# Kernel optimization log

Hardware: AMD Instinct MI355X
Metric: run time of the kernel (lower is better)

The kernel has to match this reference:

```python
import jax, jax.numpy as jnp
import numpy as np

C = 64        # channels
D = 64        # dense grid side at tensor_stride 1
N = 100000    # active voxels


def _conv3d(x, w, stride, pad):
    # x: (D,D,D,Cin), w: (kd,kh,kw,Cin,Cout) -> (D',D',D',Cout)
    return jax.lax.conv_general_dilated(
        x[None], w, window_strides=(stride,) * 3, padding=pad,
        dimension_numbers=('NDHWC', 'DHWIO', 'NDHWC'))[0]


def _sconv(x, w, b, mask, stride=1, pad='SAME'):
    # Minkowski sparse conv == dense conv on zero-filled grid, restricted to
    # the active output sites (bias only added at active sites).
    return (_conv3d(x, w, stride, pad) + b) * mask


def _forward(coords, coords_ds, feats_c1, feats_ref, w_fuse, b_fuse, w_down, b_down,
             w_conv2, b_conv2, w_p00, b_p00, w_p01, b_p01, w_p10, b_p10,
             w_p11, b_p11, w_p12, b_p12):
    dt = feats_c1.dtype
    Dh = D // 2
    ci, cj, ck = coords[:, 0], coords[:, 1], coords[:, 2]
    di, dj, dk = coords_ds[:, 0], coords_ds[:, 1], coords_ds[:, 2]
    mask = jnp.zeros((D, D, D, 1), dt).at[ci, cj, ck, 0].set(1.0)
    mask_ds = jnp.zeros((Dh, Dh, Dh, 1), dt).at[di, dj, dk, 0].set(1.0)
    fused = jnp.concatenate([feats_c1, feats_ref], axis=1)            # (N, 2C)
    x = jnp.zeros((D, D, D, 2 * C), dt).at[ci, cj, ck].set(fused)
    x = jax.nn.relu(_sconv(x, w_fuse, b_fuse, mask))                  # conv_fuse, k=3 s=1
    x = jax.nn.relu(_sconv(x, w_down, b_down, mask_ds, stride=2, pad='VALID'))  # conv_down1, k=2 s=2
    x = _sconv(x, w_conv2, b_conv2, mask_ds)                          # conv_2, no relu
    for i in range(w_p00.shape[0]):                                   # InceptionResNet x3
        p0 = jax.nn.relu(_sconv(x, w_p00[i], b_p00[i], mask_ds))      # k3 C->C/4
        p0 = _sconv(p0, w_p01[i], b_p01[i], mask_ds)                  # k3 C/4->C/2
        p1 = jax.nn.relu(_sconv(x, w_p10[i], b_p10[i], mask_ds))      # k1 C->C/4
        p1 = jax.nn.relu(_sconv(p1, w_p11[i], b_p11[i], mask_ds))     # k3 C/4->C/4
        p1 = _sconv(p1, w_p12[i], b_p12[i], mask_ds)                  # k1 C/4->C/2
        x = jnp.concatenate([p0, p1], axis=-1) + x                    # cat + residual
    return x[di, dj, dk]                                              # (M, C) sparse output feats


def setup_inputs() -> dict:
    rng = np.random.default_rng(0)
    flat = rng.choice(D ** 3, size=N, replace=False)                  # unique occupied voxels
    coords = np.stack(np.unravel_index(flat, (D, D, D)), axis=1).astype(np.int32)
    coords_ds = np.unique(coords // 2, axis=0).astype(np.int32)       # stride-2 active set
    key = jax.random.key(0)
    ks = iter(jax.random.split(key, 40))

    def W(shape, fan_in):
        return jax.random.normal(next(ks), shape, jnp.float32) / np.float32(np.sqrt(fan_in))

    def B(shape):
        return jax.random.normal(next(ks), shape, jnp.float32) * 0.01

    L = 3  # res blocks
    return dict(
        coords=jnp.asarray(coords), coords_ds=jnp.asarray(coords_ds),
        feats_c1=jax.random.normal(next(ks), (N, C), jnp.float32),
        feats_ref=jax.random.normal(next(ks), (N, C), jnp.float32),
        w_fuse=W((3, 3, 3, 2 * C, C), 27 * 2 * C), b_fuse=B((C,)),
        w_down=W((2, 2, 2, C, C), 8 * C), b_down=B((C,)),
        w_conv2=W((3, 3, 3, C, C), 27 * C), b_conv2=B((C,)),
        w_p00=W((L, 3, 3, 3, C, C // 4), 27 * C), b_p00=B((L, C // 4)),
        w_p01=W((L, 3, 3, 3, C // 4, C // 2), 27 * C // 4), b_p01=B((L, C // 2)),
        w_p10=W((L, 1, 1, 1, C, C // 4), C), b_p10=B((L, C // 4)),
        w_p11=W((L, 3, 3, 3, C // 4, C // 4), 27 * C // 4), b_p11=B((L, C // 4)),
        w_p12=W((L, 1, 1, 1, C // 4, C // 2), C // 4), b_p12=B((L, C // 2)),
    )


def reference(coords, coords_ds, feats_c1, feats_ref, w_fuse, b_fuse, w_down, b_down,
              w_conv2, b_conv2, w_p00, b_p00, w_p01, b_p01, w_p10, b_p10,
              w_p11, b_p11, w_p12, b_p12):
    return _forward(coords, coords_ds, feats_c1, feats_ref, w_fuse, b_fuse, w_down,
                    b_down, w_conv2, b_conv2, w_p00, b_p00, w_p01, b_p01, w_p10,
                    b_p10, w_p11, b_p11, w_p12, b_p12)
```

## Files before the change

kernel.cpp:

```cpp
#include <hip/hip_runtime.h>

#define GD 64
#define GDS 32

typedef _Float16 f16;
typedef __attribute__((ext_vector_type(8))) _Float16 f16x8;
typedef __attribute__((ext_vector_type(4))) float f32x4;

#define GLOAD_LDS16(SRC, DST)                                                        \
    __builtin_amdgcn_global_load_lds(                                                \
        (const __attribute__((address_space(1))) unsigned int*)(const void*)(SRC),   \
        (__attribute__((address_space(3))) unsigned int*)(void*)(DST), 16, 0, 0)

__global__ __launch_bounds__(256) void init_kernel(int* __restrict__ idx_grid,
                                                   unsigned char* __restrict__ ds_mask,
                                                   f16* __restrict__ zrow,
                                                   f16* __restrict__ f1z) {
    int i = blockIdx.x * 256 + threadIdx.x;
    if (i < GD * GD * GD) idx_grid[i] = -1;
    if (i < GDS * GDS * GDS) ds_mask[i] = 0;
    if (i < 128) zrow[i] = (f16)0.f;
    if (i < 64) f1z[i] = (f16)0.f;
}

__global__ __launch_bounds__(256) void scatter_kernel(const int* __restrict__ coords, int N,
                                                      const int* __restrict__ coords_ds, int M,
                                                      int* __restrict__ idx_grid,
                                                      unsigned char* __restrict__ ds_mask) {
    int i = blockIdx.x * 256 + threadIdx.x;
    if (i < N) {
        int a = coords[i * 3], b = coords[i * 3 + 1], c = coords[i * 3 + 2];
        idx_grid[(a * GD + b) * GD + c] = i;
    }
    if (i < M) {
        int a = coords_ds[i * 3], b = coords_ds[i * 3 + 1], c = coords_ds[i * 3 + 2];
        ds_mask[(a * GDS + b) * GDS + c] = 1;
    }
}

__global__ __launch_bounds__(256) void count_kernel(const int* __restrict__ idx_grid,
                                                    int* __restrict__ cnt) {
    __shared__ int c;
    if (threadIdx.x == 0) c = 0;
    __syncthreads();
    int s = blockIdx.x * 256 + threadIdx.x;
    bool act = idx_grid[s] >= 0;
    unsigned long long m = __ballot(act);
    if ((threadIdx.x & 63) == 0) atomicAdd(&c, __popcll(m));
    __syncthreads();
    if (threadIdx.x == 0) cnt[blockIdx.x] = c;
}

__global__ __launch_bounds__(1024) void prefix_kernel(const int* __restrict__ cnt,
                                                      int* __restrict__ off) {
    __shared__ int s[1024];
    int t = threadIdx.x;
    int v0 = cnt[t];
    s[t] = v0;
    __syncthreads();
    for (int d = 1; d < 1024; d <<= 1) {
        int v = 0;
        if (t >= d) v = s[t - d];
        __syncthreads();
        s[t] += v;
        __syncthreads();
    }
    off[t] = s[t] - v0;
}

__global__ __launch_bounds__(256) void emit_kernel(int* __restrict__ idx_grid,
                                                   const int* __restrict__ off,
                                                   int* __restrict__ sites,
                                                   int* __restrict__ perm) {
    int tid = threadIdx.x, bid = blockIdx.x;
    int s = bid * 256 + tid;
    int orig = idx_grid[s];
    bool act = orig >= 0;
    unsigned long long m = __ballot(act);
    int lane = tid & 63, wv = tid >> 6;
    __shared__ int wcnt[4];
    if (lane == 0) wcnt[wv] = __popcll(m);
    __syncthreads();
    int base = off[bid];
    for (int w = 0; w < wv; ++w) base += wcnt[w];
    int rank = __popcll(m & ((1ull << lane) - 1ull));
    if (act) {
        int q = base + rank;
        sites[q] = s;
        perm[q] = orig;
        idx_grid[s] = q;
    }
}

__global__ __launch_bounds__(256) void pack_kernel(
    const float* __restrict__ wf, const float* __restrict__ wd, const float* __restrict__ wc2,
    const float* __restrict__ wp00, const float* __restrict__ wp01, const float* __restrict__ wp10,
    const float* __restrict__ wp11, const float* __restrict__ wp12, const float* __restrict__ bp00,
    const float* __restrict__ bp01, const float* __restrict__ bp10, const float* __restrict__ bp11,
    int L, f16* __restrict__ wc1, f16* __restrict__ wdnh, f16* __restrict__ wc2h,
    f16* __restrict__ wfA, f16* __restrict__ wfB, f16* __restrict__ w12h, float* __restrict__ bA,
    float* __restrict__ bB) {
    int i = blockIdx.x * 256 + threadIdx.x;
    int n;
    n = 27 * 8192;
    if (i < n) {
        int tap = i >> 13, oc = (i >> 7) & 63, ic = i & 127;
        wc1[i] = (f16)wf[(tap * 128 + ic) * 64 + oc];
        return;
    }
    i -= n;
    n = 8 * 4096;
    if (i < n) {
        int t = i >> 12, oc = (i >> 6) & 63, ic = i & 63;
        wdnh[i] = (f16)wd[(t * 64 + ic) * 64 + oc];
        return;
    }
    i -= n;
    n = 27 * 4096;
    if (i < n) {
        int tap = i >> 12, oc = (i >> 6) & 63, ic = i & 63;
        wc2h[i] = (f16)wc2[(tap * 64 + ic) * 64 + oc];
        return;
    }
    i -= n;
    n = L * 27 * 2048;
    if (i < n) {
        int l = i / (27 * 2048), r = i - l * 27 * 2048;
        int tap = r >> 11, oc = (r >> 6) & 31, ic = r & 63;
        float v = 0.f;
        if (oc < 16) v = wp00[(((size_t)l * 27 + tap) * 64 + ic) * 16 + oc];
        else if (tap == 13) v = wp10[((size_t)l * 64 + ic) * 16 + (oc - 16)];
        wfA[i] = (f16)v;
        return;
    }
    i -= n;
    n = L * 27 * 1536;
    if (i < n) {
        int l = i / (27 * 1536), r = i - l * 27 * 1536;
        int tap = r / 1536, q = r - tap * 1536;
        int oc = q >> 5, ic = q & 31;
        float v = 0.f;
        if (oc < 32) {
            if (ic < 16) v = wp01[(((size_t)l * 27 + tap) * 16 + ic) * 32 + oc];
        } else {
            if (ic >= 16) v = wp11[(((size_t)l * 27 + tap) * 16 + (ic - 16)) * 16 + (oc - 32)];
        }
        wfB[i] = (f16)v;
        return;
    }
    i -= n;
    n = L * 512;
    if (i < n) {
        int l = i >> 9, q = i & 511, oc = q >> 4, ic = q & 15;
        w12h[i] = (f16)wp12[((size_t)l * 16 + ic) * 32 + oc];
        return;
    }
    i -= n;
    n = L * 32;
    if (i < n) {
        int l = i >> 5, oc = i & 31;
        bA[i] = (oc < 16) ? bp00[l * 16 + oc] : bp10[l * 16 + oc - 16];
        return;
    }
    i -= n;
    n = L * 48;
    if (i < n) {
        int l = i / 48, c = i - l * 48;
        bB[i] = (c < 32) ? bp01[l * 32 + c] : bp11[l * 16 + (c - 32)];
    }
}

__global__ __launch_bounds__(256) void fusef_kernel(const float* __restrict__ fc1,
                                                    const float* __restrict__ fref,
                                                    const int* __restrict__ perm, int N,
                                                    f16* __restrict__ feats) {
    int i = blockIdx.x * 256 + threadIdx.x;
    if (i < (N + 1) * 128) {
        int q = i >> 7, c = i & 127;
        float v = 0.f;
        if (q < N) {
            int p = perm[q];
            v = (c < 64) ? fc1[p * 64 + c] : fref[p * 64 + c - 64];
        }
        feats[i] = (f16)v;
    }
}

__global__ __launch_bounds__(256) void conv1_pipe(const int* __restrict__ sites,
                                                  const int* __restrict__ idx_grid, int N,
                                                  const f16* __restrict__ featsB,
                                                  const f16* __restrict__ wc1,
                                                  const float* __restrict__ bias,
                                                  f16* __restrict__ out ) {
    __shared__ f16 xb[2][64 * 128];
    __shared__ f16 wb[2][64 * 128];
    __shared__ int nbr[64 * 27];
    const int tid = threadIdx.x;
    const int nwg = gridDim.x, orig = blockIdx.x;
    const int qq = nwg >> 3, rr2 = nwg & 7;
    const int xcd = orig & 7, sub = orig >> 3;
    const int wg = (xcd < rr2 ? xcd * (qq + 1) : rr2 * (qq + 1) + (xcd - rr2) * qq) + sub;
    const int q0 = wg * 64;

    for (int t = tid; t < 64 * 27; t += 256) {
        int p = t / 27, tap = t - p * 27;
        int q = q0 + p, nb = N;
        if (q < N) {
            int s = sites[q];
            int i = (s >> 12) + tap / 9 - 1;
            int j = ((s >> 6) & 63) + (tap / 3) % 3 - 1;
            int k = (s & 63) + tap % 3 - 1;
            if ((unsigned)i < 64u && (unsigned)j < 64u && (unsigned)k < 64u) {
                int r = idx_grid[(i << 12) + (j << 6) + k];
                if (r >= 0) nb = r;
            }
        }
        nbr[t] = nb;
    }
    __syncthreads();

    const int lane = tid & 63, wid = tid >> 6;
    const int l16 = lane & 15, lq = lane >> 4;
    const int m0 = (wid >> 1) * 32, n0 = (wid & 1) * 32;

    auto STAGE = [&](int tap, int buf) {
#pragma unroll
        for (int r = 0; r < 4; ++r) {
            int slot = r * 256 + tid;
            int row = slot >> 4, cl = slot & 15;
            int c = cl ^ (row & 15);
            const f16* src = featsB + (size_t)nbr[row * 27 + tap] * 128 + c * 8;
            GLOAD_LDS16(src, &xb[buf][0] + (size_t)(r * 256 + (tid & ~63)) * 8);
        }
#pragma unroll
        for (int r = 0; r < 4; ++r) {
            int slot = r * 256 + tid;
            int row = slot >> 4, cl = slot & 15;
            int c = cl ^ (row & 15);
            const f16* src = wc1 + (size_t)((tap * 64 + row) * 128 + c * 8);
            GLOAD_LDS16(src, &wb[buf][0] + (size_t)(r * 256 + (tid & ~63)) * 8);
        }
    };

    f32x4 acc[2][2] = {};
    STAGE(0, 0);
    STAGE(1, 1);
    for (int tap = 0; tap < 27; ++tap) {
        if (tap < 26) {
            asm volatile("s_waitcnt vmcnt(8)" ::: "memory");
        } else {
            asm volatile("s_waitcnt vmcnt(0)" ::: "memory");
        }
        __builtin_amdgcn_sched_barrier(0);
        __builtin_amdgcn_s_barrier();

        const f16* xp = &xb[tap & 1][0];
        const f16* wp = &wb[tap & 1][0];
        f16x8 a[2][4], b[2][4];
#pragma unroll
        for (int mi = 0; mi < 2; ++mi) {
            int row = m0 + mi * 16 + l16;
#pragma unroll
            for (int ks = 0; ks < 4; ++ks)
                a[mi][ks] =
                    *(const f16x8*)(xp + (size_t)row * 128 + (size_t)((((ks * 4 + lq) ^ l16)) * 8));
        }
#pragma unroll
        for (int ni = 0; ni < 2; ++ni) {
            int col = n0 + ni * 16 + l16;
#pragma unroll
            for (int ks = 0; ks < 4; ++ks)
                b[ni][ks] =
                    *(const f16x8*)(wp + (size_t)col * 128 + (size_t)((((ks * 4 + lq) ^ l16)) * 8));
        }
#pragma unroll
        for (int mi = 0; mi < 2; ++mi)
#pragma unroll
            for (int ni = 0; ni < 2; ++ni)
#pragma unroll
                for (int ks = 0; ks < 4; ++ks)
                    acc[mi][ni] = __builtin_amdgcn_mfma_f32_16x16x32_f16(a[mi][ks], b[ni][ks],
                                                                         acc[mi][ni], 0, 0, 0);
        asm volatile("s_waitcnt lgkmcnt(0)" ::: "memory");
        __builtin_amdgcn_sched_barrier(0);
        __builtin_amdgcn_s_barrier();
        if (tap + 2 < 27) STAGE(tap + 2, tap & 1);
    }

#pragma unroll
    for (int ni = 0; ni < 2; ++ni) {
        int col = n0 + ni * 16 + l16;
        float bv = bias[col];
#pragma unroll
        for (int mi = 0; mi < 2; ++mi) {
#pragma unroll
            for (int j = 0; j < 4; ++j) {
                int q = q0 + m0 + mi * 16 + lq * 4 + j;
                if (q < N) {
                    float v = acc[mi][ni][j] + bv;
                    out[(size_t)q * 64 + col] = (f16)(v > 0.f ? v : 0.f);
                }
            }
        }
    }
}

__global__ __launch_bounds__(512) void down_mfma(const f16* __restrict__ feats1h, int N,
                                                 const int* __restrict__ idx_grid,
                                                 const f16* __restrict__ wdn,
                                                 const float* __restrict__ bias,
                                                 const unsigned char* __restrict__ mask,
                                                 f16* __restrict__ out ) {
    __shared__ f16 xs[2][128 * 64];
    __shared__ f16 wl[2][512 * 8];
    __shared__ int nbr[128 * 8];
    const int tid = threadIdx.x;
    const int s0 = blockIdx.x * 128;
    for (int t = tid; t < 128 * 8; t += 512) {
        int sl = t >> 3, tp = t & 7;
        int s = s0 + sl;
        int i = s >> 10, j = (s >> 5) & 31, k = s & 31;
        int ci = 2 * i + (tp >> 2), cj = 2 * j + ((tp >> 1) & 1), ck = 2 * k + (tp & 1);
        int r = idx_grid[(ci * GD + cj) * GD + ck];
        nbr[t] = (r >= 0) ? r : N;
    }
    __syncthreads();
    auto STAGEX = [&](int tp, int buf) {
#pragma unroll
        for (int rr = 0; rr < 2; ++rr) {
            int slot = rr * 512 + tid;
            int row = slot >> 3, cl = slot & 7;
            int c = cl ^ (row & 7);
            const f16* src = feats1h + (size_t)nbr[row * 8 + tp] * 64 + c * 8;
            GLOAD_LDS16(src, &xs[buf][0] + (size_t)(rr * 512 + (tid & ~63)) * 8);
        }
    };
    auto STAGEW = [&](int tp, int buf) {
        int row = tid >> 3, cl = tid & 7;
        int c = cl ^ (row & 7);
        const f16* src = wdn + (size_t)((tp * 64 + row) * 64 + c * 8);
        GLOAD_LDS16(src, &wl[buf][0] + (size_t)(tid & ~63) * 8);
    };
    const int lane = tid & 63, wid = tid >> 6;
    const int l16 = lane & 15, lq = lane >> 4;
    const int wm = wid >> 1, wn = wid & 1;
    const int m0 = wm * 32, n0 = wn * 32;
    f32x4 acc[2][2] = {};
    STAGEX(0, 0);
    STAGEW(0, 0);
    STAGEX(1, 1);
    STAGEW(1, 1);
    for (int tp = 0; tp < 8; ++tp) {
        if (tp < 7) {
            asm volatile("s_waitcnt vmcnt(3)" ::: "memory");
        } else {
            asm volatile("s_waitcnt vmcnt(0)" ::: "memory");
        }
        __builtin_amdgcn_sched_barrier(0);
        __builtin_amdgcn_s_barrier();
        const f16* xbp = &xs[tp & 1][0];
        const f16* wbp = &wl[tp & 1][0];
        f16x8 a[2][2], bfr[2][2];
#pragma unroll
        for (int mi = 0; mi < 2; ++mi) {
            int row = m0 + mi * 16 + l16;
#pragma unroll
            for (int ks = 0; ks < 2; ++ks) {
                int ch = ks * 4 + lq;
                a[mi][ks] = *(const f16x8*)(xbp + (size_t)row * 64 + (ch ^ (row & 7)) * 8);
            }
        }
#pragma unroll
        for (int ni = 0; ni < 2; ++ni) {
            int col = n0 + ni * 16 + l16;
#pragma unroll
            for (int ks = 0; ks < 2; ++ks) {
                int ch = ks * 4 + lq;
                bfr[ni][ks] = *(const f16x8*)(wbp + (size_t)col * 64 + (ch ^ (col & 7)) * 8);
            }
        }
#pragma unroll
        for (int mi = 0; mi < 2; ++mi)
#pragma unroll
            for (int ni = 0; ni < 2; ++ni)
#pragma unroll
                for (int ks = 0; ks < 2; ++ks)
                    acc[mi][ni] = __builtin_amdgcn_mfma_f32_16x16x32_f16(a[mi][ks], bfr[ni][ks],
                                                                         acc[mi][ni], 0, 0, 0);
        asm volatile("s_waitcnt lgkmcnt(0)" ::: "memory");
        __builtin_amdgcn_sched_barrier(0);
        __builtin_amdgcn_s_barrier();
        if (tp + 2 < 8) {
            STAGEX(tp + 2, tp & 1);
            STAGEW(tp + 2, tp & 1);
        }
    }
#pragma unroll
    for (int mi = 0; mi < 2; ++mi) {
        int m = m0 + mi * 16 + lq * 4;
        int site = s0 + m;
        unsigned mword = *(const unsigned*)(mask + site);
#pragma unroll
        for (int ni = 0; ni < 2; ++ni) {
            int col = n0 + ni * 16 + l16;
            float bv = bias[col];
#pragma unroll
            for (int j = 0; j < 4; ++j) {
                float v = 0.f;
                if ((mword >> (8 * j)) & 255) {
                    v = acc[mi][ni][j] + bv;
                    v = v > 0.f ? v : 0.f;
                }
                out[(size_t)(site + j) * 64 + col] = (f16)v;
            }
        }
    }
}

template <int CIN, int COUT, int NW, int RELUFROM>
__global__ __launch_bounds__(512) void dconv_kernel(const f16* __restrict__ x,
                                                    const f16* __restrict__ wp,
                                                    const float* __restrict__ bias,
                                                    const unsigned char* __restrict__ mask,
                                                    const f16* __restrict__ zrow,
                                                    f16* __restrict__ out, int ostr) {
    constexpr int NCH = CIN / 8;
    constexpr int PSLOT = 34 * NCH;
    constexpr int STOT = 18 * PSLOT;
    constexpr int RNDS = (STOT + 511) / 512;
    constexpr int MW = 8 / NW;
    constexpr int WM = 128 / MW, WN = COUT / NW;
    constexpr int FM = WM / 16, FN = WN / 16, KS = CIN / 32;
    constexpr int WSLOTS = COUT * NCH;
    __shared__ f16 xs[RNDS * 512 * 8];
    __shared__ f16 wl[2][512 * 8];

    const int tid = threadIdx.x;
    const int bid = blockIdx.x;
    const int i0 = bid >> 3, j0 = (bid & 7) * 4;

    for (int rr = 0; rr < RNDS; ++rr) {
        int slot = rr * 512 + tid;
        int p = slot / PSLOT;
        int rem = slot - p * PSLOT;
        int r = rem / NCH;
        int cl = rem - r * NCH;
        int c = cl ^ (r & (NCH - 1));
        int gi = i0 + p / 6 - 1, gj = j0 + p % 6 - 1, gk = r - 1;
        bool ok = (slot < STOT) && ((unsigned)gi < 32u) && ((unsigned)gj < 32u) &&
                  ((unsigned)gk < 32u);
        const f16* src = ok ? (x + (size_t)(((gi * 32 + gj) * 32 + gk) * CIN + c * 8)) : zrow;
        f16* dst = xs + (size_t)(rr * 512 + (tid & ~63)) * 8;
        GLOAD_LDS16(src, dst);
    }
    auto STAGEW = [&](int tap, int buf) {
        int row = tid / NCH, cl = tid % NCH;
        int c = cl ^ (row & (NCH - 1));
        const f16* src = (tid < WSLOTS) ? (wp + (size_t)((tap * COUT + row) * CIN + c * 8)) : wp;
        GLOAD_LDS16(src, &wl[buf][0] + (size_t)(tid & ~63) * 8);
    };
    STAGEW(0, 0);
    STAGEW(1, 1);

    const int lane = tid & 63, wid = tid >> 6;
    const int l16 = lane & 15, lq = lane >> 4;
    const int wm = wid / NW, wn = wid - wm * NW;
    const int m0 = wm * WM, n0 = wn * WN;

    f32x4 acc[FM][FN] = {};

    for (int tap = 0; tap < 27; ++tap) {
        if (tap < 26) {
            asm volatile("s_waitcnt vmcnt(1)" ::: "memory");
        } else {
            asm volatile("s_waitcnt vmcnt(0)" ::: "memory");
        }
        __builtin_amdgcn_sched_barrier(0);
        __builtin_amdgcn_s_barrier();

        int di = tap / 9 - 1, dj = (tap / 3) % 3 - 1, dk = tap % 3 - 1;
        const f16* wbp = &wl[tap & 1][0];
        f16x8 a[FM][KS], bfr[FN][KS];
#pragma unroll
        for (int mi = 0; mi < FM; ++mi) {
            int m = m0 + mi * 16 + l16;
            int pj = m >> 5, k = m & 31;
            int p = (di + 1) * 6 + (pj + dj + 1);
            int r = k + dk + 1;
#pragma unroll
            for (int ks = 0; ks < KS; ++ks) {
                int ch = ks * 4 + lq;
                a[mi][ks] =
                    *(const f16x8*)(xs + (size_t)(p * PSLOT + r * NCH + (ch ^ (r & (NCH - 1)))) * 8);
            }
        }
#pragma unroll
        for (int ni = 0; ni < FN; ++ni) {
            int col = n0 + ni * 16 + l16;
#pragma unroll
            for (int ks = 0; ks < KS; ++ks) {
                int ch = ks * 4 + lq;
                bfr[ni][ks] =
                    *(const f16x8*)(wbp + (size_t)(col * NCH + (ch ^ (col & (NCH - 1)))) * 8);
            }
        }
#pragma unroll
        for (int mi = 0; mi < FM; ++mi)
#pragma unroll
            for (int ni = 0; ni < FN; ++ni)
#pragma unroll
                for (int ks = 0; ks < KS; ++ks)
                    acc[mi][ni] = __builtin_amdgcn_mfma_f32_16x16x32_f16(a[mi][ks], bfr[ni][ks],
                                                                         acc[mi][ni], 0, 0, 0);
        asm volatile("s_waitcnt lgkmcnt(0)" ::: "memory");
        __builtin_amdgcn_sched_barrier(0);
        __builtin_amdgcn_s_barrier();
        if (tap + 2 < 27) STAGEW(tap + 2, tap & 1);
    }

#pragma unroll
    for (int mi = 0; mi < FM; ++mi) {
        int m = m0 + mi * 16 + lq * 4;
        int pj = m >> 5, k = m & 31;
        int gsite = ((i0 * 32) + (j0 + pj)) * 32 + k;
        unsigned mword = *(const unsigned*)(mask + gsite);
#pragma unroll
        for (int ni = 0; ni < FN; ++ni) {
            int col = n0 + ni * 16 + l16;
            float bv = bias[col];
#pragma unroll
            for (int j = 0; j < 4; ++j) {
                float v = 0.f;
                if ((mword >> (8 * j)) & 255) {
                    v = acc[mi][ni][j] + bv;
                    if (col >= RELUFROM) v = v > 0.f ? v : 0.f;
                }
                out[(size_t)(gsite + j) * ostr + col] = (f16)v;
            }
        }
    }
}

template <typename OUTT>
__global__ __launch_bounds__(256) void tail_kernel(const f16* __restrict__ ph,
                                                   const f16* __restrict__ xh,
                                                   const f16* __restrict__ w12,
                                                   const float* __restrict__ b12,
                                                   const unsigned char* __restrict__ mask,
                                                   OUTT* __restrict__ y ) {
    __shared__ float ws[512];
    __shared__ float bs[32];
    int tid = threadIdx.x;
    ws[tid] = (float)w12[tid];
    ws[tid + 256] = (float)w12[tid + 256];
    if (tid < 32) bs[tid] = b12[tid];
    __syncthreads();
    int g = tid >> 6, lane = tid & 63;
    int site = blockIdx.x * 64 + lane;
    const f16x8* pr = (const f16x8*)(ph + (size_t)site * 64);
    const f16x8* xr = (const f16x8*)(xh + (size_t)site * 64);
    float yv[16];
    int col0;
    if (g < 2) {
        col0 = g * 16;
        f16x8 p0 = pr[g * 2], p1 = pr[g * 2 + 1];
        f16x8 x0 = xr[g * 2], x1 = xr[g * 2 + 1];
#pragma unroll
        for (int j = 0; j < 8; ++j) {
            yv[j] = (float)p0[j] + (float)x0[j];
            yv[8 + j] = (float)p1[j] + (float)x1[j];
        }
    } else {
        int oc0 = (g - 2) * 16;
        col0 = 32 + oc0;
        f16x8 u0 = pr[4], u1 = pr[5];
        float u[16];
#pragma unroll
        for (int j = 0; j < 8; ++j) {
            u[j] = (float)u0[j];
            u[8 + j] = (float)u1[j];
        }
        f16x8 x0 = xr[4 + (g - 2) * 2], x1 = xr[5 + (g - 2) * 2];
        bool mk = mask[site] != 0;
#pragma unroll
        for (int oc = 0; oc < 16; ++oc) {
            float s = 0.f;
#pragma unroll
            for (int ic = 0; ic < 16; ++ic) s += u[ic] * ws[(oc0 + oc) * 16 + ic];
            float p1v = mk ? (s + bs[oc0 + oc]) : 0.f;
            yv[oc] = p1v + (float)((oc < 8) ? x0[oc] : x1[oc - 8]);
        }
    }
#pragma unroll
    for (int j = 0; j < 16; ++j) y[(size_t)site * 64 + col0 + j] = (OUTT)yv[j];
}

__global__ __launch_bounds__(256) void gather_kernel(const float* __restrict__ x,
                                                     const int* __restrict__ coords_ds, int M,
                                                     float* __restrict__ out) {
    int i = blockIdx.x * 256 + threadIdx.x;
    if (i < M * 64) {
        int m = i >> 6, oc = i & 63;
        int a = coords_ds[m * 3], b = coords_ds[m * 3 + 1], c = coords_ds[m * 3 + 2];
        out[i] = x[((size_t)((a * GDS + b) * GDS + c) << 6) + oc];
    }
}

extern "C" void kernel_launch(void* const* d_in, const int* in_sizes, int n_in,
                              void* d_out, int out_size, void* d_ws, size_t ws_size,
                              hipStream_t stream) {
    const int* coords = (const int*)d_in[0];
    const int* coords_ds = (const int*)d_in[1];
    const float* fc1 = (const float*)d_in[2];
    const float* fref = (const float*)d_in[3];
    const float* w_fuse = (const float*)d_in[4];
    const float* b_fuse = (const float*)d_in[5];
    const float* w_down = (const float*)d_in[6];
    const float* b_down = (const float*)d_in[7];
    const float* w_conv2 = (const float*)d_in[8];
    const float* b_conv2 = (const float*)d_in[9];
    const float* w_p00 = (const float*)d_in[10];
    const float* b_p00 = (const float*)d_in[11];
    const float* w_p01 = (const float*)d_in[12];
    const float* b_p01 = (const float*)d_in[13];
    const float* w_p10 = (const float*)d_in[14];
    const float* b_p10 = (const float*)d_in[15];
    const float* w_p11 = (const float*)d_in[16];
    const float* b_p11 = (const float*)d_in[17];
    const float* w_p12 = (const float*)d_in[18];
    const float* b_p12 = (const float*)d_in[19];

    const int N = in_sizes[0] / 3;
    const int M = in_sizes[1] / 3;
    const int L = in_sizes[10] / (27 * 64 * 16);
    const int NSITES = GDS * GDS * GDS;

    size_t off = 0;
    auto alloc = [&](size_t bytes) {
        void* p = (char*)d_ws + off;
        off += (bytes + 255) & ~(size_t)255;
        return p;
    };
    int* idx_grid = (int*)alloc((size_t)GD * GD * GD * 4);
    unsigned char* ds_mask = (unsigned char*)alloc(NSITES);
    f16* zrow = (f16*)alloc(256);
    int* chunk_cnt = (int*)alloc(1024 * 4);
    int* chunk_off = (int*)alloc(1024 * 4);
    int* sites = (int*)alloc((size_t)N * 4);
    int* perm = (int*)alloc((size_t)N * 4);
    f16* featsB = (f16*)alloc((size_t)(N + 1) * 128 * 2);
    f16* feats1h = (f16*)alloc((size_t)(N + 1) * 64 * 2);
    f16* xdown = (f16*)alloc((size_t)NSITES * 64 * 2);
    f16* x0 = (f16*)alloc((size_t)NSITES * 64 * 2);
    f16* y1 = (f16*)alloc((size_t)NSITES * 64 * 2);
    f16* y2 = (f16*)alloc((size_t)NSITES * 64 * 2);
    f16* thh = (f16*)alloc((size_t)NSITES * 32 * 2);
    f16* ph = (f16*)alloc((size_t)NSITES * 64 * 2);
    float* xF = (float*)alloc((size_t)NSITES * 64 * 4);
    f16* wc1 = (f16*)alloc((size_t)27 * 8192 * 2);
    f16* wdnh = (f16*)alloc((size_t)8 * 4096 * 2);
    f16* wc2h = (f16*)alloc((size_t)27 * 4096 * 2);
    f16* wfA = (f16*)alloc((size_t)L * 27 * 2048 * 2);
    f16* wfB = (f16*)alloc((size_t)L * 27 * 1536 * 2);
    f16* w12h = (f16*)alloc((size_t)L * 512 * 2);
    float* bA = (float*)alloc((size_t)L * 32 * 4);
    float* bB = (float*)alloc((size_t)L * 48 * 4);
    (void)ws_size;

    float* out = (float*)d_out;
    (void)out_size;
    (void)n_in;

    init_kernel<<<(GD * GD * GD + 255) / 256, 256, 0, stream>>>(idx_grid, ds_mask, zrow,
                                                                feats1h + (size_t)N * 64);
    {
        int mx = N > M ? N : M;
        scatter_kernel<<<(mx + 255) / 256, 256, 0, stream>>>(coords, N, coords_ds, M, idx_grid,
                                                             ds_mask);
    }
    count_kernel<<<1024, 256, 0, stream>>>(idx_grid, chunk_cnt);
    prefix_kernel<<<1, 1024, 0, stream>>>(chunk_cnt, chunk_off);
    emit_kernel<<<1024, 256, 0, stream>>>(idx_grid, chunk_off, sites, perm);
    {
        int tot = 27 * 8192 + 8 * 4096 + 27 * 4096 + L * 27 * 2048 + L * 27 * 1536 + L * 512 +
                  L * 32 + L * 48;
        pack_kernel<<<(tot + 255) / 256, 256, 0, stream>>>(
            w_fuse, w_down, w_conv2, w_p00, w_p01, w_p10, w_p11, w_p12, b_p00, b_p01, b_p10, b_p11,
            L, wc1, wdnh, wc2h, wfA, wfB, w12h, bA, bB);
    }
    fusef_kernel<<<((N + 1) * 128 + 255) / 256, 256, 0, stream>>>(fc1, fref, perm, N, featsB);

    conv1_pipe<<<(N + 63) / 64, 256, 0, stream>>>(sites, idx_grid, N, featsB, wc1, b_fuse,
                                                  feats1h);
    down_mfma<<<NSITES / 128, 512, 0, stream>>>(feats1h, N, idx_grid, wdnh, b_down, ds_mask,
                                                xdown);
    dconv_kernel<64, 64, 2, 64>
        <<<256, 512, 0, stream>>>(xdown, wc2h, b_conv2, ds_mask, zrow, x0, 64);

    f16* x = x0;
    for (int l = 0; l < L; ++l) {
        dconv_kernel<64, 32, 2, 0>
            <<<256, 512, 0, stream>>>(x, wfA + (size_t)l * 27 * 2048, bA + l * 32, ds_mask, zrow,
                                      thh, 32);
        dconv_kernel<32, 48, 1, 32>
            <<<256, 512, 0, stream>>>(thh, wfB + (size_t)l * 27 * 1536, bB + l * 48, ds_mask, zrow,
                                      ph, 64);
        if (l < L - 1) {
            f16* yn = (l == 0) ? y1 : y2;
            tail_kernel<f16><<<NSITES / 64, 256, 0, stream>>>(ph, x, w12h + (size_t)l * 512,
                                                              b_p12 + l * 32, ds_mask, yn);
            x = yn;
        } else {
            tail_kernel<float><<<NSITES / 64, 256, 0, stream>>>(ph, x, w12h + (size_t)l * 512,
                                                                b_p12 + l * 32, ds_mask, xF);
        }
    }

    gather_kernel<<<(M * 64 + 255) / 256, 256, 0, stream>>>(xF, coords_ds, M, out);
}
```

Measured before the change: 292.3 us.

## Split conv1 taps across two wave groups and merge init with weight packing

conv1_pipe now runs 512 threads per block. Two 4-wave groups take alternating taps, one on each double-buffer slot, and their partial accumulators are combined through LDS before bias and ReLU. This aims to overlap staging and MFMA work across groups and to halve each thread's load count. It adds an LDS reduction and an extra barrier, and each group sits idle on every other tap. Separately, the grid init and weight packing kernels are merged into one launch to save a kernel launch.

```diff
diff --git a/kernel.cpp b/kernel.cpp
--- a/kernel.cpp
+++ b/kernel.cpp
@@ -12,15 +12,89 @@
         (const __attribute__((address_space(1))) unsigned int*)(const void*)(SRC),   \
         (__attribute__((address_space(3))) unsigned int*)(void*)(DST), 16, 0, 0)
 
-__global__ __launch_bounds__(256) void init_kernel(int* __restrict__ idx_grid,
-                                                   unsigned char* __restrict__ ds_mask,
-                                                   f16* __restrict__ zrow,
-                                                   f16* __restrict__ f1z) {
-    int i = blockIdx.x * 256 + threadIdx.x;
-    if (i < GD * GD * GD) idx_grid[i] = -1;
-    if (i < GDS * GDS * GDS) ds_mask[i] = 0;
-    if (i < 128) zrow[i] = (f16)0.f;
-    if (i < 64) f1z[i] = (f16)0.f;
+__global__ __launch_bounds__(256) void init_pack_kernel(
+    int* __restrict__ idx_grid, unsigned char* __restrict__ ds_mask, f16* __restrict__ zrow,
+    f16* __restrict__ f1z, const float* __restrict__ wf, const float* __restrict__ wd,
+    const float* __restrict__ wc2, const float* __restrict__ wp00, const float* __restrict__ wp01,
+    const float* __restrict__ wp10, const float* __restrict__ wp11, const float* __restrict__ wp12,
+    const float* __restrict__ bp00, const float* __restrict__ bp01, const float* __restrict__ bp10,
+    const float* __restrict__ bp11, int L, f16* __restrict__ wc1, f16* __restrict__ wdnh,
+    f16* __restrict__ wc2h, f16* __restrict__ wfA, f16* __restrict__ wfB, f16* __restrict__ w12h,
+    float* __restrict__ bA, float* __restrict__ bB) {
+    int i0 = blockIdx.x * 256 + threadIdx.x;
+    if (i0 < GD * GD * GD) idx_grid[i0] = -1;
+    if (i0 < GDS * GDS * GDS) ds_mask[i0] = 0;
+    if (i0 < 128) zrow[i0] = (f16)0.f;
+    if (i0 < 64) f1z[i0] = (f16)0.f;
+
+    int i = i0;
+    int n;
+    n = 27 * 8192;
+    if (i < n) {
+        int tap = i >> 13, oc = (i >> 7) & 63, ic = i & 127;
+        wc1[i] = (f16)wf[(tap * 128 + ic) * 64 + oc];
+        return;
+    }
+    i -= n;
+    n = 8 * 4096;
+    if (i < n) {
+        int t = i >> 12, oc = (i >> 6) & 63, ic = i & 63;
+        wdnh[i] = (f16)wd[(t * 64 + ic) * 64 + oc];
+        return;
+    }
+    i -= n;
+    n = 27 * 4096;
+    if (i < n) {
+        int tap = i >> 12, oc = (i >> 6) & 63, ic = i & 63;
+        wc2h[i] = (f16)wc2[(tap * 64 + ic) * 64 + oc];
+        return;
+    }
+    i -= n;
+    n = L * 27 * 2048;
+    if (i < n) {
+        int l = i / (27 * 2048), r = i - l * 27 * 2048;
+        int tap = r >> 11, oc = (r >> 6) & 31, ic = r & 63;
+        float v = 0.f;
+        if (oc < 16) v = wp00[(((size_t)l * 27 + tap) * 64 + ic) * 16 + oc];
+        else if (tap == 13) v = wp10[((size_t)l * 64 + ic) * 16 + (oc - 16)];
+        wfA[i] = (f16)v;
+        return;
+    }
+    i -= n;
+    n = L * 27 * 1536;
+    if (i < n) {
+        int l = i / (27 * 1536), r = i - l * 27 * 1536;
+        int tap = r / 1536, q = r - tap * 1536;
+        int oc = q >> 5, ic = q & 31;
+        float v = 0.f;
+        if (oc < 32) {
+            if (ic < 16) v = wp01[(((size_t)l * 27 + tap) * 16 + ic) * 32 + oc];
+        } else {
+            if (ic >= 16) v = wp11[(((size_t)l * 27 + tap) * 16 + (ic - 16)) * 16 + (oc - 32)];
+        }
+        wfB[i] = (f16)v;
+        return;
+    }
+    i -= n;
+    n = L * 512;
+    if (i < n) {
+        int l = i >> 9, q = i & 511, oc = q >> 4, ic = q & 15;
+        w12h[i] = (f16)wp12[((size_t)l * 16 + ic) * 32 + oc];
+        return;
+    }
+    i -= n;
+    n = L * 32;
+    if (i < n) {
+        int l = i >> 5, oc = i & 31;
+        bA[i] = (oc < 16) ? bp00[l * 16 + oc] : bp10[l * 16 + oc - 16];
+        return;
+    }
+    i -= n;
+    n = L * 48;
+    if (i < n) {
+        int l = i / 48, c = i - l * 48;
+        bB[i] = (c < 32) ? bp01[l * 32 + c] : bp11[l * 16 + (c - 32)];
+    }
 }
 
 __global__ __launch_bounds__(256) void scatter_kernel(const int* __restrict__ coords, int N,
@@ -92,84 +166,6 @@
     }
 }
 
-__global__ __launch_bounds__(256) void pack_kernel(
-    const float* __restrict__ wf, const float* __restrict__ wd, const float* __restrict__ wc2,
-    const float* __restrict__ wp00, const float* __restrict__ wp01, const float* __restrict__ wp10,
-    const float* __restrict__ wp11, const float* __restrict__ wp12, const float* __restrict__ bp00,
-    const float* __restrict__ bp01, const float* __restrict__ bp10, const float* __restrict__ bp11,
-    int L, f16* __restrict__ wc1, f16* __restrict__ wdnh, f16* __restrict__ wc2h,
-    f16* __restrict__ wfA, f16* __restrict__ wfB, f16* __restrict__ w12h, float* __restrict__ bA,
-    float* __restrict__ bB) {
-    int i = blockIdx.x * 256 + threadIdx.x;
-    int n;
-    n = 27 * 8192;
-    if (i < n) {
-        int tap = i >> 13, oc = (i >> 7) & 63, ic = i & 127;
-        wc1[i] = (f16)wf[(tap * 128 + ic) * 64 + oc];
-        return;
-    }
-    i -= n;
-    n = 8 * 4096;
-    if (i < n) {
-        int t = i >> 12, oc = (i >> 6) & 63, ic = i & 63;
-        wdnh[i] = (f16)wd[(t * 64 + ic) * 64 + oc];
-        return;
-    }
-    i -= n;
-    n = 27 * 4096;
-    if (i < n) {
-        int tap = i >> 12, oc = (i >> 6) & 63, ic = i & 63;
-        wc2h[i] = (f16)wc2[(tap * 64 + ic) * 64 + oc];
-        return;
-    }
-    i -= n;
-    n = L * 27 * 2048;
-    if (i < n) {
-        int l = i / (27 * 2048), r = i - l * 27 * 2048;
-        int tap = r >> 11, oc = (r >> 6) & 31, ic = r & 63;
-        float v = 0.f;
-        if (oc < 16) v = wp00[(((size_t)l * 27 + tap) * 64 + ic) * 16 + oc];
-        else if (tap == 13) v = wp10[((size_t)l * 64 + ic) * 16 + (oc - 16)];
-        wfA[i] = (f16)v;
-        return;
-    }
-    i -= n;
-    n = L * 27 * 1536;
-    if (i < n) {
-        int l = i / (27 * 1536), r = i - l * 27 * 1536;
-        int tap = r / 1536, q = r - tap * 1536;
-        int oc = q >> 5, ic = q & 31;
-        float v = 0.f;
-        if (oc < 32) {
-            if (ic < 16) v = wp01[(((size_t)l * 27 + tap) * 16 + ic) * 32 + oc];
-        } else {
-            if (ic >= 16) v = wp11[(((size_t)l * 27 + tap) * 16 + (ic - 16)) * 16 + (oc - 32)];
-        }
-        wfB[i] = (f16)v;
-        return;
-    }
-    i -= n;
-    n = L * 512;
-    if (i < n) {
-        int l = i >> 9, q = i & 511, oc = q >> 4, ic = q & 15;
-        w12h[i] = (f16)wp12[((size_t)l * 16 + ic) * 32 + oc];
-        return;
-    }
-    i -= n;
-    n = L * 32;
-    if (i < n) {
-        int l = i >> 5, oc = i & 31;
-        bA[i] = (oc < 16) ? bp00[l * 16 + oc] : bp10[l * 16 + oc - 16];
-        return;
-    }
-    i -= n;
-    n = L * 48;
-    if (i < n) {
-        int l = i / 48, c = i - l * 48;
-        bB[i] = (c < 32) ? bp01[l * 32 + c] : bp11[l * 16 + (c - 32)];
-    }
-}
-
 __global__ __launch_bounds__(256) void fusef_kernel(const float* __restrict__ fc1,
                                                     const float* __restrict__ fref,
                                                     const int* __restrict__ perm, int N,
@@ -186,7 +182,7 @@
     }
 }
 
-__global__ __launch_bounds__(256) void conv1_pipe(const int* __restrict__ sites,
+__global__ __launch_bounds__(512) void conv1_pipe(const int* __restrict__ sites,
                                                   const int* __restrict__ idx_grid, int N,
                                                   const f16* __restrict__ featsB,
                                                   const f16* __restrict__ wc1,
@@ -202,7 +198,7 @@
     const int wg = (xcd < rr2 ? xcd * (qq + 1) : rr2 * (qq + 1) + (xcd - rr2) * qq) + sub;
     const int q0 = wg * 64;
 
-    for (int t = tid; t < 64 * 27; t += 256) {
+    for (int t = tid; t < 64 * 27; t += 512) {
         int p = t / 27, tap = t - p * 27;
         int q = q0 + p, nb = N;
         if (q < N) {
@@ -221,24 +217,25 @@
 
     const int lane = tid & 63, wid = tid >> 6;
     const int l16 = lane & 15, lq = lane >> 4;
-    const int m0 = (wid >> 1) * 32, n0 = (wid & 1) * 32;
+    const int grp = wid >> 2, w4 = wid & 3;
+    const int m0 = (w4 >> 1) * 32, n0 = (w4 & 1) * 32;
 
     auto STAGE = [&](int tap, int buf) {
 #pragma unroll
-        for (int r = 0; r < 4; ++r) {
-            int slot = r * 256 + tid;
+        for (int r = 0; r < 2; ++r) {
+            int slot = r * 512 + tid;
             int row = slot >> 4, cl = slot & 15;
             int c = cl ^ (row & 15);
             const f16* src = featsB + (size_t)nbr[row * 27 + tap] * 128 + c * 8;
-            GLOAD_LDS16(src, &xb[buf][0] + (size_t)(r * 256 + (tid & ~63)) * 8);
-        }
-#pragma unroll
-        for (int r = 0; r < 4; ++r) {
-            int slot = r * 256 + tid;
+            GLOAD_LDS16(src, &xb[buf][0] + (size_t)(r * 512 + (tid & ~63)) * 8);
+        }
+#pragma unroll
+        for (int r = 0; r < 2; ++r) {
+            int slot = r * 512 + tid;
             int row = slot >> 4, cl = slot & 15;
             int c = cl ^ (row & 15);
             const f16* src = wc1 + (size_t)((tap * 64 + row) * 128 + c * 8);
-            GLOAD_LDS16(src, &wb[buf][0] + (size_t)(r * 256 + (tid & ~63)) * 8);
+            GLOAD_LDS16(src, &wb[buf][0] + (size_t)(r * 512 + (tid & ~63)) * 8);
         }
     };
 
@@ -247,58 +244,74 @@
     STAGE(1, 1);
     for (int tap = 0; tap < 27; ++tap) {
         if (tap < 26) {
-            asm volatile("s_waitcnt vmcnt(8)" ::: "memory");
+            asm volatile("s_waitcnt vmcnt(4)" ::: "memory");
         } else {
             asm volatile("s_waitcnt vmcnt(0)" ::: "memory");
         }
         __builtin_amdgcn_sched_barrier(0);
         __builtin_amdgcn_s_barrier();
 
-        const f16* xp = &xb[tap & 1][0];
-        const f16* wp = &wb[tap & 1][0];
-        f16x8 a[2][4], b[2][4];
-#pragma unroll
-        for (int mi = 0; mi < 2; ++mi) {
-            int row = m0 + mi * 16 + l16;
-#pragma unroll
-            for (int ks = 0; ks < 4; ++ks)
-                a[mi][ks] =
-                    *(const f16x8*)(xp + (size_t)row * 128 + (size_t)((((ks * 4 + lq) ^ l16)) * 8));
-        }
-#pragma unroll
-        for (int ni = 0; ni < 2; ++ni) {
-            int col = n0 + ni * 16 + l16;
-#pragma unroll
-            for (int ks = 0; ks < 4; ++ks)
-                b[ni][ks] =
-                    *(const f16x8*)(wp + (size_t)col * 128 + (size_t)((((ks * 4 + lq) ^ l16)) * 8));
-        }
-#pragma unroll
-        for (int mi = 0; mi < 2; ++mi)
-#pragma unroll
-            for (int ni = 0; ni < 2; ++ni)
+        if (grp == (tap & 1)) {
+            const f16* xp = &xb[tap & 1][0];
+            const f16* wp = &wb[tap & 1][0];
+            f16x8 a[2][4], b[2][4];
+#pragma unroll
+            for (int mi = 0; mi < 2; ++mi) {
+                int row = m0 + mi * 16 + l16;
 #pragma unroll
                 for (int ks = 0; ks < 4; ++ks)
-                    acc[mi][ni] = __builtin_amdgcn_mfma_f32_16x16x32_f16(a[mi][ks], b[ni][ks],
-                                                                         acc[mi][ni], 0, 0, 0);
+                    a[mi][ks] = *(const f16x8*)(xp + (size_t)row * 128 +
+                                                (size_t)((((ks * 4 + lq) ^ l16)) * 8));
+            }
+#pragma unroll
+            for (int ni = 0; ni < 2; ++ni) {
+                int col = n0 + ni * 16 + l16;
+#pragma unroll
+                for (int ks = 0; ks < 4; ++ks)
+                    b[ni][ks] = *(const f16x8*)(wp + (size_t)col * 128 +
+                                                (size_t)((((ks * 4 + lq) ^ l16)) * 8));
+            }
+#pragma unroll
+            for (int mi = 0; mi < 2; ++mi)
+#pragma unroll
+                for (int ni = 0; ni < 2; ++ni)
+#pragma unroll
+                    for (int ks = 0; ks < 4; ++ks)
+                        acc[mi][ni] = __builtin_amdgcn_mfma_f32_16x16x32_f16(a[mi][ks], b[ni][ks],
+                                                                             acc[mi][ni], 0, 0, 0);
+        }
         asm volatile("s_waitcnt lgkmcnt(0)" ::: "memory");
         __builtin_amdgcn_sched_barrier(0);
         __builtin_amdgcn_s_barrier();
         if (tap + 2 < 27) STAGE(tap + 2, tap & 1);
     }
 
-#pragma unroll
-    for (int ni = 0; ni < 2; ++ni) {
-        int col = n0 + ni * 16 + l16;
-        float bv = bias[col];
-#pragma unroll
-        for (int mi = 0; mi < 2; ++mi) {
-#pragma unroll
-            for (int j = 0; j < 4; ++j) {
-                int q = q0 + m0 + mi * 16 + lq * 4 + j;
-                if (q < N) {
-                    float v = acc[mi][ni][j] + bv;
-                    out[(size_t)q * 64 + col] = (f16)(v > 0.f ? v : 0.f);
+    float* red = (float*)&xb[0][0];
+    if (grp == 1) {
+#pragma unroll
+        for (int mi = 0; mi < 2; ++mi)
+#pragma unroll
+            for (int ni = 0; ni < 2; ++ni)
+#pragma unroll
+                for (int j = 0; j < 4; ++j)
+                    red[(m0 + mi * 16 + lq * 4 + j) * 65 + n0 + ni * 16 + l16] = acc[mi][ni][j];
+    }
+    __syncthreads();
+    if (grp == 0) {
+#pragma unroll
+        for (int ni = 0; ni < 2; ++ni) {
+            int col = n0 + ni * 16 + l16;
+            float bv = bias[col];
+#pragma unroll
+            for (int mi = 0; mi < 2; ++mi) {
+#pragma unroll
+                for (int j = 0; j < 4; ++j) {
+                    int row = m0 + mi * 16 + lq * 4 + j;
+                    int q = q0 + row;
+                    if (q < N) {
+                        float v = acc[mi][ni][j] + red[row * 65 + col] + bv;
+                        out[(size_t)q * 64 + col] = (f16)(v > 0.f ? v : 0.f);
+                    }
                 }
             }
         }
@@ -671,8 +684,15 @@
     (void)out_size;
     (void)n_in;
 
-    init_kernel<<<(GD * GD * GD + 255) / 256, 256, 0, stream>>>(idx_grid, ds_mask, zrow,
-                                                                feats1h + (size_t)N * 64);
+    {
+        int tot = 27 * 8192 + 8 * 4096 + 27 * 4096 + L * 27 * 2048 + L * 27 * 1536 + L * 512 +
+                  L * 32 + L * 48;
+        if (tot < GD * GD * GD) tot = GD * GD * GD;
+        init_pack_kernel<<<(tot + 255) / 256, 256, 0, stream>>>(
+            idx_grid, ds_mask, zrow, feats1h + (size_t)N * 64, w_fuse, w_down, w_conv2, w_p00,
+            w_p01, w_p10, w_p11, w_p12, b_p00, b_p01, b_p10, b_p11, L, wc1, wdnh, wc2h, wfA, wfB,
+            w12h, bA, bB);
+    }
     {
         int mx = N > M ? N : M;
         scatter_kernel<<<(mx + 255) / 256, 256, 0, stream>>>(coords, N, coords_ds, M, idx_grid,
@@ -681,16 +701,9 @@
     count_kernel<<<1024, 256, 0, stream>>>(idx_grid, chunk_cnt);
     prefix_kernel<<<1, 1024, 0, stream>>>(chunk_cnt, chunk_off);
     emit_kernel<<<1024, 256, 0, stream>>>(idx_grid, chunk_off, sites, perm);
-    {
-        int tot = 27 * 8192 + 8 * 4096 + 27 * 4096 + L * 27 * 2048 + L * 27 * 1536 + L * 512 +
-                  L * 32 + L * 48;
-        pack_kernel<<<(tot + 255) / 256, 256, 0, stream>>>(
-            w_fuse, w_down, w_conv2, w_p00, w_p01, w_p10, w_p11, w_p12, b_p00, b_p01, b_p10, b_p11,
-            L, wc1, wdnh, wc2h, wfA, wfB, w12h, bA, bB);
-    }
     fusef_kernel<<<((N + 1) * 128 + 255) / 256, 256, 0, stream>>>(fc1, fref, perm, N, featsB);
 
-    conv1_pipe<<<(N + 63) / 64, 256, 0, stream>>>(sites, idx_grid, N, featsB, wc1, b_fuse,
+    conv1_pipe<<<(N + 63) / 64, 512, 0, stream>>>(sites, idx_grid, N, featsB, wc1, b_fuse,
                                                   feats1h);
     down_mfma<<<NSITES / 128, 512, 0, stream>>>(feats1h, N, idx_grid, wdnh, b_down, ds_mask,
                                                 xdown);
```

Measured after the change: 274.3 us. -6.1%, faster.
